# Kernel optimization log

Hardware: AMD Instinct MI355X
Metric: run time of the kernel (lower is better)

## Reference

```python
import jax, jax.numpy as jnp
import numpy as np

NUM_EXPERTS = 8
TOP_K = 2


def setup_inputs() -> dict:
    key = jax.random.key(0)
    ks = jax.random.split(key, 8)
    B = 16384
    D = 1024
    feat0 = jax.random.normal(ks[0], (B, 768), dtype=jnp.float32)
    feat1 = jax.random.normal(ks[1], (B, 512), dtype=jnp.float32)
    feat2 = jax.random.normal(ks[2], (B, 256), dtype=jnp.float32)
    # parameters (scaled like torch default init ~1/sqrt(fan_in))
    W_shared = jax.random.normal(ks[3], (1536, D), dtype=jnp.float32) * (1.0 / np.sqrt(1536))
    b_shared = jnp.zeros((D,), dtype=jnp.float32)
    W_gate = jax.random.normal(ks[4], (D, NUM_EXPERTS), dtype=jnp.float32) * (1.0 / np.sqrt(D))
    b_gate = jnp.zeros((NUM_EXPERTS,), dtype=jnp.float32)
    W_experts = jax.random.normal(ks[5], (NUM_EXPERTS, D, D), dtype=jnp.float32) * (1.0 / np.sqrt(D))
    b_experts = jnp.zeros((NUM_EXPERTS, D), dtype=jnp.float32)
    return {
        "feat0": feat0, "feat1": feat1, "feat2": feat2,
        "W_shared": W_shared, "b_shared": b_shared,
        "W_gate": W_gate, "b_gate": b_gate,
        "W_experts": W_experts, "b_experts": b_experts,
    }


def _moe_forward(feat0, feat1, feat2, W_shared, b_shared, W_gate, b_gate, W_experts, b_experts):
    x = jnp.concatenate([feat0, feat1, feat2], axis=1)          # (B, sum_d)
    h = jax.nn.gelu(x @ W_shared + b_shared, approximate=False)  # (B, D)
    gate_probs = jax.nn.softmax(h @ W_gate + b_gate, axis=-1)    # (B, E)
    topk_probs, topk_idx = jax.lax.top_k(gate_probs, TOP_K)      # (B, K)
    out = jnp.zeros_like(h)
    for e in range(NUM_EXPERTS):
        # per-token combine weight for expert e (0 if not routed to e)
        w_e = jnp.sum(topk_probs * (topk_idx == e), axis=1)      # (B,)
        expert_out = jax.nn.gelu(h @ W_experts[e] + b_experts[e], approximate=False)
        out = out + w_e[:, None] * expert_out
    return out


def reference(feat0, feat1, feat2, W_shared, b_shared, W_gate, b_gate, W_experts, b_experts):
    return _moe_forward(feat0, feat1, feat2, W_shared, b_shared, W_gate, b_gate, W_experts, b_experts)
```

## Files before the change

kernel.cpp:

```cpp
#include <hip/hip_runtime.h>
#include <math.h>

#define NB_TOK 16384
#define DM     1024
#define NEXP   8
#define KIN    1536
#define SECBIT 0x40000000
#define TOKMSK 0x3FFFFFFF

typedef __attribute__((ext_vector_type(8))) short          short8;
typedef __attribute__((ext_vector_type(8))) unsigned short ushort8;
typedef __attribute__((ext_vector_type(4))) unsigned short ushort4v;
typedef __attribute__((ext_vector_type(8))) _Float16       half8;
typedef __attribute__((ext_vector_type(4))) float          floatx4;

#define AS1U(p) ((const __attribute__((address_space(1))) unsigned int*)(p))
#define AS3U(p) ((__attribute__((address_space(3))) unsigned int*)(p))

__device__ __forceinline__ float gelu_f(float x) {
    return 0.5f * x * (1.0f + erff(x * 0.70710678118654752440f));
}

__device__ __forceinline__ unsigned short f2bf(float x) {
    unsigned u = __float_as_uint(x);
    u = (u + 0x7FFF + ((u >> 16) & 1)) >> 16;
    return (unsigned short)u;
}

__device__ __forceinline__ void split_h16(float x, unsigned short& hi, unsigned short& lo) {
    _Float16 h = (_Float16)x;
    float r = x - (float)h;
    _Float16 l = (_Float16)r;
    hi = *(unsigned short*)&h;
    lo = *(unsigned short*)&l;
}

__global__ __launch_bounds__(256) void k_splitA(
    const float* __restrict__ f0, const float* __restrict__ f1,
    const float* __restrict__ f2, unsigned short* __restrict__ Ah,
    unsigned short* __restrict__ Al)
{
    const int i4  = blockIdx.x * 256 + threadIdx.x;
    const int tok = i4 / (KIN / 4);
    const int k   = (i4 % (KIN / 4)) * 4;
    const float* src; int ld, c;
    if (k < 768)       { src = f0; ld = 768; c = k; }
    else if (k < 1280) { src = f1; ld = 512; c = k - 768; }
    else               { src = f2; ld = 256; c = k - 1280; }
    const float4 v = *(const float4*)(src + (size_t)tok * ld + c);
    const float* vp = (const float*)&v;
    ushort4v hi, lo;
#pragma unroll
    for (int j = 0; j < 4; ++j) {
        unsigned short h, l;
        split_h16(vp[j] * 4.0f, h, l);
        hi[j] = h; lo[j] = l;
    }
    *(ushort4v*)(Ah + (size_t)tok * KIN + k) = hi;
    *(ushort4v*)(Al + (size_t)tok * KIN + k) = lo;
}

__global__ __launch_bounds__(256) void k_splitB(
    const float* __restrict__ Ws, unsigned short* __restrict__ BhT,
    unsigned short* __restrict__ BlT)
{
    __shared__ float s[32][33];
    const int n0 = blockIdx.x * 32, k0 = blockIdx.y * 32;
    const int c  = threadIdx.x & 31, r = threadIdx.x >> 5;
#pragma unroll
    for (int p = 0; p < 4; ++p)
        s[r + p * 8][c] = Ws[(size_t)(k0 + r + p * 8) * DM + n0 + c];
    __syncthreads();
#pragma unroll
    for (int p = 0; p < 4; ++p) {
        const int n = r + p * 8;
        unsigned short h, l;
        split_h16(s[c][n] * 256.0f, h, l);
        BhT[(size_t)(n0 + n) * KIN + k0 + c] = h;
        BlT[(size_t)(n0 + n) * KIN + k0 + c] = l;
    }
}

__global__ __launch_bounds__(256) void k_shared_mfma(
    const unsigned short* __restrict__ Ah, const unsigned short* __restrict__ Al,
    const unsigned short* __restrict__ BhT, const unsigned short* __restrict__ BlT,
    const float* __restrict__ bs, float* __restrict__ h)
{
    __shared__ unsigned short ldsAh[128][64];
    __shared__ unsigned short ldsAl[128][64];
    __shared__ unsigned short ldsBh[128][64];
    __shared__ unsigned short ldsBl[128][64];

    const int t    = threadIdx.x;
    const int lane = t & 63;
    const int wave = t >> 6;
    const int bid  = blockIdx.x;
    const int brow = ((bid >> 6) << 3) + (bid & 7);
    const int bcol = (bid >> 3) & 7;
    const int row0 = brow * 128;
    const int n0g  = bcol * 128;

    const int srow = t >> 3;
    const int g    = (t & 7) ^ (srow & 7);
    const unsigned short *sAh[4], *sAl[4], *sBh[4], *sBl[4];
#pragma unroll
    for (int q = 0; q < 4; ++q) {
        const size_t ra = (size_t)(row0 + q * 32 + srow) * KIN + g * 8;
        const size_t rb = (size_t)(n0g + q * 32 + srow) * KIN + g * 8;
        sAh[q] = Ah + ra; sAl[q] = Al + ra;
        sBh[q] = BhT + rb; sBl[q] = BlT + rb;
    }

    const int grp = lane >> 4;
    int offA[2][4], offB[2][4];
#pragma unroll
    for (int ks = 0; ks < 2; ++ks)
#pragma unroll
        for (int m = 0; m < 4; ++m) {
            const int rA = ((wave >> 1) * 64) + m * 16 + (lane & 15);
            const int rB = ((wave & 1) * 64) + m * 16 + (lane & 15);
            const int c  = ks * 4 + grp;
            offA[ks][m] = rA * 128 + (((c ^ (rA & 7)) & 7) << 4);
            offB[ks][m] = rB * 128 + (((c ^ (rB & 7)) & 7) << 4);
        }

    floatx4 acc[4][4];
#pragma unroll
    for (int m = 0; m < 4; ++m)
#pragma unroll
        for (int n = 0; n < 4; ++n) acc[m][n] = (floatx4){0.f, 0.f, 0.f, 0.f};

    const char* lAh = (const char*)&ldsAh[0][0];
    const char* lAl = (const char*)&ldsAl[0][0];
    const char* lBh = (const char*)&ldsBh[0][0];
    const char* lBl = (const char*)&ldsBl[0][0];

    for (int kt = 0; kt < KIN / 64; ++kt) {
        const int k0 = kt * 64;
        __syncthreads();
#pragma unroll
        for (int q = 0; q < 4; ++q) {
            const int dst = q * 4096 + wave * 1024;
            __builtin_amdgcn_global_load_lds(AS1U(sAh[q] + k0), AS3U((char*)lAh + dst), 16, 0, 0);
            __builtin_amdgcn_global_load_lds(AS1U(sAl[q] + k0), AS3U((char*)lAl + dst), 16, 0, 0);
            __builtin_amdgcn_global_load_lds(AS1U(sBh[q] + k0), AS3U((char*)lBh + dst), 16, 0, 0);
            __builtin_amdgcn_global_load_lds(AS1U(sBl[q] + k0), AS3U((char*)lBl + dst), 16, 0, 0);
        }
        __syncthreads();
#pragma unroll
        for (int ks = 0; ks < 2; ++ks) {
            half8 ah[4], al[4], bh[4], bl[4];
#pragma unroll
            for (int m = 0; m < 4; ++m) {
                ah[m] = *(const half8*)(lAh + offA[ks][m]);
                al[m] = *(const half8*)(lAl + offA[ks][m]);
            }
#pragma unroll
            for (int n = 0; n < 4; ++n) {
                bh[n] = *(const half8*)(lBh + offB[ks][n]);
                bl[n] = *(const half8*)(lBl + offB[ks][n]);
            }
#pragma unroll
            for (int m = 0; m < 4; ++m)
#pragma unroll
                for (int n = 0; n < 4; ++n) {
                    acc[m][n] = __builtin_amdgcn_mfma_f32_16x16x32_f16(ah[m], bh[n], acc[m][n], 0, 0, 0);
                    acc[m][n] = __builtin_amdgcn_mfma_f32_16x16x32_f16(ah[m], bl[n], acc[m][n], 0, 0, 0);
                    acc[m][n] = __builtin_amdgcn_mfma_f32_16x16x32_f16(al[m], bh[n], acc[m][n], 0, 0, 0);
                }
        }
    }

    const int wr = wave >> 1, wc = wave & 1;
#pragma unroll
    for (int n = 0; n < 4; ++n) {
        const int col  = n0g + wc * 64 + n * 16 + (lane & 15);
        const float bias = bs[col];
#pragma unroll
        for (int m = 0; m < 4; ++m) {
            const int rbase = row0 + wr * 64 + m * 16 + (lane >> 4) * 4;
#pragma unroll
            for (int reg = 0; reg < 4; ++reg) {
                const float o = gelu_f(acc[m][n][reg] * (1.0f / 1024.0f) + bias);
                h[(size_t)(rbase + reg) * DM + col] = o;
            }
        }
    }
}

__global__ __launch_bounds__(256) void k_wt_bf16(
    const float* __restrict__ We, unsigned short* __restrict__ WeT)
{
    __shared__ float s[32][33];
    const int e  = blockIdx.z;
    const int k0 = blockIdx.y * 32, n0 = blockIdx.x * 32;
    const int c  = threadIdx.x & 31, r = threadIdx.x >> 5;
    const float* W = We + ((size_t)e << 20);
#pragma unroll
    for (int p = 0; p < 4; ++p) {
        const int k = r + p * 8;
        s[k][c] = W[(size_t)(k0 + k) * DM + n0 + c];
    }
    __syncthreads();
#pragma unroll
    for (int p = 0; p < 4; ++p) {
        const int n = r + p * 8;
        WeT[((size_t)e << 20) + (size_t)(n0 + n) * DM + k0 + c] = f2bf(s[c][n]);
    }
}

__global__ __launch_bounds__(256) void k_gate_topk(
    const float* __restrict__ h, const float* __restrict__ Wg,
    const float* __restrict__ bg, int* __restrict__ eidx,
    float2* __restrict__ w01)
{
    const int lane = threadIdx.x & 63;
    const int wv   = threadIdx.x >> 6;
    const int tok  = blockIdx.x * 4 + wv;
    const float* hr = h + (size_t)tok * DM;
    float acc[NEXP];
#pragma unroll
    for (int e = 0; e < NEXP; ++e) acc[e] = 0.f;
    for (int j = 0; j < DM / 64; ++j) {
        const float hv = hr[lane + 64 * j];
        const float* wr = Wg + (size_t)(lane + 64 * j) * NEXP;
#pragma unroll
        for (int e = 0; e < NEXP; ++e) acc[e] = fmaf(hv, wr[e], acc[e]);
    }
#pragma unroll
    for (int off = 32; off > 0; off >>= 1) {
#pragma unroll
        for (int e = 0; e < NEXP; ++e) acc[e] += __shfl_xor(acc[e], off, 64);
    }
    if (lane == 0) {
        float lg[NEXP];
        float mx = -1e30f;
#pragma unroll
        for (int e = 0; e < NEXP; ++e) { lg[e] = acc[e] + bg[e]; mx = fmaxf(mx, lg[e]); }
        float p[NEXP]; float s = 0.f;
#pragma unroll
        for (int e = 0; e < NEXP; ++e) { p[e] = expf(lg[e] - mx); s += p[e]; }
        const float inv = 1.f / s;
        int i0 = 0;
#pragma unroll
        for (int e = 1; e < NEXP; ++e) if (p[e] > p[i0]) i0 = e;
        int i1 = (i0 == 0) ? 1 : 0;
#pragma unroll
        for (int e = 0; e < NEXP; ++e) if (e != i0 && p[e] > p[i1]) i1 = e;
        eidx[tok] = i0 | (i1 << 8);
        w01[tok]  = make_float2(p[i0] * inv, p[i1] * inv);
    }
}

__global__ __launch_bounds__(256) void k_bucket(
    const int* __restrict__ eidx, const float2* __restrict__ w01,
    int* __restrict__ counts, int* __restrict__ btok, float* __restrict__ bwgt)
{
    __shared__ int lcnt[NEXP], lbase[NEXP];
    const int tid = threadIdx.x;
    const int tok = blockIdx.x * 256 + tid;
    if (tid < NEXP) lcnt[tid] = 0;
    __syncthreads();
    const int ee = eidx[tok];
    const float2 w = w01[tok];
    const int e0 = ee & 0xff, e1 = ee >> 8;
    const int l0 = atomicAdd(&lcnt[e0], 1);
    const int l1 = atomicAdd(&lcnt[e1], 1);
    __syncthreads();
    if (tid < NEXP) lbase[tid] = atomicAdd(&counts[tid], lcnt[tid]);
    __syncthreads();
    const int s0 = lbase[e0] + l0;
    btok[e0 * NB_TOK + s0] = tok;           bwgt[e0 * NB_TOK + s0] = w.x;
    const int s1 = lbase[e1] + l1;
    btok[e1 * NB_TOK + s1] = tok | SECBIT;  bwgt[e1 * NB_TOK + s1] = w.y;
}

__global__ void k_prefix(const int* __restrict__ counts, int* __restrict__ basep)
{
    if (threadIdx.x == 0) {
        int r = 0;
#pragma unroll
        for (int e = 0; e < NEXP; ++e) { basep[e] = r; r += counts[e]; }
    }
}

__global__ __launch_bounds__(256) void k_gather(
    const float* __restrict__ h, const int* __restrict__ btok,
    const int* __restrict__ basep, unsigned short* __restrict__ hbfc)
{
    const int g = blockIdx.x;
    int e = 0;
#pragma unroll
    for (int i = 1; i < NEXP; ++i) if (g >= basep[i]) e = i;
    const int idx = g - basep[e];
    const int tok = btok[e * NB_TOK + idx] & TOKMSK;
    const int c   = threadIdx.x * 4;
    const float4 v = *(const float4*)(h + (size_t)tok * DM + c);
    ushort4v o;
    o[0] = f2bf(v.x); o[1] = f2bf(v.y); o[2] = f2bf(v.z); o[3] = f2bf(v.w);
    *(ushort4v*)(hbfc + (size_t)g * DM + c) = o;
}

#define EXP_STAGE(b, k0)                                                                              \
    {                                                                                                 \
        char* lAw = (char*)&ldsA[b][0][0];                                                            \
        char* lBw = (char*)&ldsB[b][0][0];                                                            \
        _Pragma("unroll")                                                                             \
        for (int q = 0; q < 4; ++q) {                                                                 \
            __builtin_amdgcn_global_load_lds(AS1U(srcA[q] + (k0)), AS3U(lAw + q * 4096 + wave * 1024), 16, 0, 0); \
            __builtin_amdgcn_global_load_lds(AS1U(srcB[q] + (k0)), AS3U(lBw + q * 4096 + wave * 1024), 16, 0, 0); \
        }                                                                                             \
    }

__global__ __launch_bounds__(256) void k_expert_mfma(
    const unsigned short* __restrict__ hbfc,
    const unsigned short* __restrict__ WeT,
    const float* __restrict__ bexp,
    const int* __restrict__ counts, const int* __restrict__ basep,
    const int* __restrict__ btok, const float* __restrict__ bwgt,
    float* __restrict__ stage2, float* __restrict__ out)
{
    const int e    = blockIdx.z;
    const int cnt  = counts[e];
    const int row0 = blockIdx.y * 128;
    if (row0 >= cnt) return;
    const int gb   = basep[e];

    __shared__ unsigned short ldsA[2][128][64];
    __shared__ unsigned short ldsB[2][128][64];
    __shared__ int   sTok[128];
    __shared__ float sWt[128];

    const int t    = threadIdx.x;
    const int lane = t & 63;
    const int wave = t >> 6;

    const int srow = t >> 3;
    const int g    = (t & 7) ^ (srow & 7);
    const int n0g  = blockIdx.x * 128;
    const unsigned short* srcA[4];
    const unsigned short* srcB[4];
#pragma unroll
    for (int q = 0; q < 4; ++q) {
        srcA[q] = hbfc + (size_t)(gb + row0 + q * 32 + srow) * DM + g * 8;
        srcB[q] = WeT + ((size_t)e << 20) + (size_t)(n0g + q * 32 + srow) * DM + g * 8;
    }

    EXP_STAGE(0, 0);

    if (t < 128) {
        const int idx = row0 + t;
        if (idx < cnt) { sTok[t] = btok[e * NB_TOK + idx]; sWt[t] = bwgt[e * NB_TOK + idx]; }
        else           { sTok[t] = 0;                      sWt[t] = 0.f; }
    }

    const int grp = lane >> 4;
    int offA[2][4], offB[2][4];
#pragma unroll
    for (int ks = 0; ks < 2; ++ks)
#pragma unroll
        for (int m = 0; m < 4; ++m) {
            const int rA = ((wave >> 1) * 64) + m * 16 + (lane & 15);
            const int rB = ((wave & 1) * 64) + m * 16 + (lane & 15);
            const int c  = ks * 4 + grp;
            offA[ks][m] = rA * 128 + (((c ^ (rA & 7)) & 7) << 4);
            offB[ks][m] = rB * 128 + (((c ^ (rB & 7)) & 7) << 4);
        }

    floatx4 acc[4][4];
#pragma unroll
    for (int m = 0; m < 4; ++m)
#pragma unroll
        for (int n = 0; n < 4; ++n) acc[m][n] = (floatx4){0.f, 0.f, 0.f, 0.f};

    int buf = 0;
    for (int kt = 0; kt < DM / 64; ++kt) {
        __syncthreads();
        if (kt + 1 < DM / 64) EXP_STAGE(buf ^ 1, (kt + 1) * 64);
        const char* lA = (const char*)&ldsA[buf][0][0];
        const char* lB = (const char*)&ldsB[buf][0][0];
#pragma unroll
        for (int ks = 0; ks < 2; ++ks) {
            short8 av[4], bv[4];
#pragma unroll
            for (int m = 0; m < 4; ++m) av[m] = *(const short8*)(lA + offA[ks][m]);
#pragma unroll
            for (int n = 0; n < 4; ++n) bv[n] = *(const short8*)(lB + offB[ks][n]);
#pragma unroll
            for (int m = 0; m < 4; ++m)
#pragma unroll
                for (int n = 0; n < 4; ++n)
                    acc[m][n] = __builtin_amdgcn_mfma_f32_16x16x32_bf16(av[m], bv[n], acc[m][n], 0, 0, 0);
        }
        buf ^= 1;
    }

    const int wr = wave >> 1, wc = wave & 1;
#pragma unroll
    for (int n = 0; n < 4; ++n) {
        const int col  = n0g + wc * 64 + n * 16 + (lane & 15);
        const float bias = bexp[e * DM + col];
#pragma unroll
        for (int m = 0; m < 4; ++m) {
            const int rbase = wr * 64 + m * 16 + (lane >> 4) * 4;
#pragma unroll
            for (int reg = 0; reg < 4; ++reg) {
                const int r = rbase + reg;
                if (row0 + r >= cnt) continue;
                const int raw = sTok[r];
                const int tok = raw & TOKMSK;
                const float v = gelu_f(acc[m][n][reg] + bias) * sWt[r];
                float* dst = (raw & SECBIT) ? stage2 : out;
                dst[(size_t)tok * DM + col] = v;
            }
        }
    }
}

__global__ __launch_bounds__(256) void k_combine(
    const float* __restrict__ stage2, float* __restrict__ out)
{
    const int tok = blockIdx.x;
    const int c   = threadIdx.x * 4;
    const float4 a = *(const float4*)(out    + (size_t)tok * DM + c);
    const float4 b = *(const float4*)(stage2 + (size_t)tok * DM + c);
    float4 o;
    o.x = a.x + b.x; o.y = a.y + b.y; o.z = a.z + b.z; o.w = a.w + b.w;
    *(float4*)(out + (size_t)tok * DM + c) = o;
}

extern "C" void kernel_launch(void* const* d_in, const int* in_sizes, int n_in,
                              void* d_out, int out_size, void* d_ws, size_t ws_size,
                              hipStream_t stream)
{
    const float* f0 = (const float*)d_in[0];
    const float* f1 = (const float*)d_in[1];
    const float* f2 = (const float*)d_in[2];
    const float* Ws = (const float*)d_in[3];
    const float* bs = (const float*)d_in[4];
    const float* Wg = (const float*)d_in[5];
    const float* bg = (const float*)d_in[6];
    const float* We = (const float*)d_in[7];
    const float* be = (const float*)d_in[8];
    float* out = (float*)d_out;

    const size_t MB = 1048576ULL;
    char* base = (char*)d_ws;
    unsigned short* Ah    = (unsigned short*)(base);
    unsigned short* Al    = (unsigned short*)(base + 48 * MB);
    unsigned short* BhT   = (unsigned short*)(base + 96 * MB);
    unsigned short* BlT   = (unsigned short*)(base + 99 * MB);
    float*          h     = (float*)(base + 102 * MB);
    unsigned short* WeT   = (unsigned short*)(base + 2 * MB);
    unsigned short* hbfc  = (unsigned short*)(base + 18 * MB);
    float*          stage2= (float*)(base + 82 * MB);
    int*    counts = (int*)(base);
    int*    basep  = counts + 16;
    int*    btok   = counts + 64;
    float*  bwgt   = (float*)(btok + NEXP * NB_TOK);
    int*    eidx   = (int*)(bwgt + NEXP * NB_TOK);
    float2* w01    = (float2*)(eidx + NB_TOK);

    k_splitA<<<NB_TOK * (KIN / 4) / 256, 256, 0, stream>>>(f0, f1, f2, Ah, Al);
    k_splitB<<<dim3(DM / 32, KIN / 32), 256, 0, stream>>>(Ws, BhT, BlT);
    k_shared_mfma<<<1024, 256, 0, stream>>>(Ah, Al, BhT, BlT, bs, h);

    hipMemsetAsync(counts, 0, 16 * sizeof(int), stream);
    k_gate_topk<<<NB_TOK / 4, 256, 0, stream>>>(h, Wg, bg, eidx, w01);
    k_bucket<<<NB_TOK / 256, 256, 0, stream>>>(eidx, w01, counts, btok, bwgt);
    k_prefix<<<1, 64, 0, stream>>>(counts, basep);
    k_gather<<<2 * NB_TOK, 256, 0, stream>>>(h, btok, basep, hbfc);

    k_wt_bf16<<<dim3(DM / 32, DM / 32, NEXP), 256, 0, stream>>>(We, WeT);

    k_expert_mfma<<<dim3(DM / 128, NB_TOK / 128, NEXP), 256, 0, stream>>>(
        hbfc, WeT, be, counts, basep, btok, bwgt, stage2, out);
    k_combine<<<NB_TOK, 256, 0, stream>>>(stage2, out);
}
```

Baseline: 491.1 us.

## Single-buffer expert GEMM LDS and replace erff with polynomial GELU

The expert MFMA kernel drops its double-buffered LDS tiles for a single buffer. Each next tile is loaded only after a barrier that follows the current compute step. This halves LDS use per block, which may let more blocks run per CU, but the global-to-LDS load no longer overlaps with the MFMA work inside a block. GELU's erff is also replaced by the Abramowitz-Stegun polynomial with a fast exp, which cuts epilogue math at the cost of roughly 1e-7 absolute erf error.

Measured after the change: 416.9 us. -15.1%, faster.

```diff
diff --git a/kernel.cpp b/kernel.cpp
--- a/kernel.cpp
+++ b/kernel.cpp
@@ -18,7 +18,17 @@
 #define AS3U(p) ((__attribute__((address_space(3))) unsigned int*)(p))
 
 __device__ __forceinline__ float gelu_f(float x) {
-    return 0.5f * x * (1.0f + erff(x * 0.70710678118654752440f));
+    const float ax = fabsf(x) * 0.70710678118654752440f;
+    const float t  = 1.0f / fmaf(0.3275911f, ax, 1.0f);
+    float p = fmaf(t, 1.061405429f, -1.453152027f);
+    p = fmaf(t, p, 1.421413741f);
+    p = fmaf(t, p, -0.284496736f);
+    p = fmaf(t, p, 0.254829592f);
+    p = p * t;
+    const float e = __expf(-ax * ax);
+    float erf = fmaf(-p, e, 1.0f);
+    erf = copysignf(erf, x);
+    return 0.5f * x * (1.0f + erf);
 }
 
 __device__ __forceinline__ unsigned short f2bf(float x) {
@@ -301,10 +311,10 @@
     *(ushort4v*)(hbfc + (size_t)g * DM + c) = o;
 }
 
-#define EXP_STAGE(b, k0)                                                                              \
+#define EXP_STAGE(k0)                                                                                 \
     {                                                                                                 \
-        char* lAw = (char*)&ldsA[b][0][0];                                                            \
-        char* lBw = (char*)&ldsB[b][0][0];                                                            \
+        char* lAw = (char*)&ldsA[0][0];                                                               \
+        char* lBw = (char*)&ldsB[0][0];                                                               \
         _Pragma("unroll")                                                                             \
         for (int q = 0; q < 4; ++q) {                                                                 \
             __builtin_amdgcn_global_load_lds(AS1U(srcA[q] + (k0)), AS3U(lAw + q * 4096 + wave * 1024), 16, 0, 0); \
@@ -326,8 +336,8 @@
     if (row0 >= cnt) return;
     const int gb   = basep[e];
 
-    __shared__ unsigned short ldsA[2][128][64];
-    __shared__ unsigned short ldsB[2][128][64];
+    __shared__ unsigned short ldsA[128][64];
+    __shared__ unsigned short ldsB[128][64];
     __shared__ int   sTok[128];
     __shared__ float sWt[128];
 
@@ -346,7 +356,7 @@
         srcB[q] = WeT + ((size_t)e << 20) + (size_t)(n0g + q * 32 + srow) * DM + g * 8;
     }
 
-    EXP_STAGE(0, 0);
+    EXP_STAGE(0);
 
     if (t < 128) {
         const int idx = row0 + t;
@@ -373,12 +383,11 @@
 #pragma unroll
         for (int n = 0; n < 4; ++n) acc[m][n] = (floatx4){0.f, 0.f, 0.f, 0.f};
 
-    int buf = 0;
+    const char* lA = (const char*)&ldsA[0][0];
+    const char* lB = (const char*)&ldsB[0][0];
+
     for (int kt = 0; kt < DM / 64; ++kt) {
         __syncthreads();
-        if (kt + 1 < DM / 64) EXP_STAGE(buf ^ 1, (kt + 1) * 64);
-        const char* lA = (const char*)&ldsA[buf][0][0];
-        const char* lB = (const char*)&ldsB[buf][0][0];
 #pragma unroll
         for (int ks = 0; ks < 2; ++ks) {
             short8 av[4], bv[4];
@@ -392,7 +401,10 @@
                 for (int n = 0; n < 4; ++n)
                     acc[m][n] = __builtin_amdgcn_mfma_f32_16x16x32_bf16(av[m], bv[n], acc[m][n], 0, 0, 0);
         }
-        buf ^= 1;
+        if (kt + 1 < DM / 64) {
+            __syncthreads();
+            EXP_STAGE((kt + 1) * 64);
+        }
     }
 
     const int wr = wave >> 1, wc = wave & 1;
```
